# Optimization experiments

Measured on AMD Instinct MI355X. Metric: run time of the kernel, lower is better.

Reference implementation:

```python
import jax, jax.numpy as jnp
import numpy as np

N_HEADS = 16
D_MODEL = 2048
DK = D_MODEL // N_HEADS
SEQ = 2048


def setup_inputs() -> dict:
    key = jax.random.key(0)
    ks = jax.random.split(key, 11)
    s = 0.02
    return {
        "query": jax.random.normal(ks[0], (SEQ, D_MODEL), jnp.float32),
        "key": jax.random.normal(ks[1], (SEQ, D_MODEL), jnp.float32),
        "value": jax.random.normal(ks[2], (SEQ, D_MODEL), jnp.float32),
        # per-head projection weights, stacked over heads: [H, d_model, dk]
        "Wq": jax.random.normal(ks[3], (N_HEADS, D_MODEL, DK), jnp.float32) * s,
        "bq": jnp.zeros((N_HEADS, DK), jnp.float32),
        "Wk": jax.random.normal(ks[4], (N_HEADS, D_MODEL, DK), jnp.float32) * s,
        "bk": jnp.zeros((N_HEADS, DK), jnp.float32),
        "Wv": jax.random.normal(ks[5], (N_HEADS, D_MODEL, DK), jnp.float32) * s,
        "bv": jnp.zeros((N_HEADS, DK), jnp.float32),
        # output projection: [H*dk, d_model]
        "Wo": jax.random.normal(ks[6], (N_HEADS * DK, D_MODEL), jnp.float32) * s,
        "bo": jnp.zeros((D_MODEL,), jnp.float32),
    }


def reference(query, key, value, Wq, bq, Wk, bk, Wv, bv, Wo, bo):
    # Per-head linear projections, batched over heads. q/k/v: [H, S, dk]
    q = jnp.einsum('sd,hdk->hsk', query, Wq) + bq[:, None, :]
    k = jnp.einsum('sd,hdk->hsk', key, Wk) + bk[:, None, :]
    v = jnp.einsum('sd,hdk->hsk', value, Wv) + bv[:, None, :]
    scale = jnp.sqrt(jnp.asarray(DK, q.dtype))
    # scores: [H, S_q, S_k]
    scores = jnp.einsum('hsk,htk->hst', q, k) / scale
    # Faithful to original: Softmax(dim=0) on each 2D [S_q, S_k] matrix
    # -> normalize over the QUERY axis (axis=1 here).
    attn = jax.nn.softmax(scores, axis=1)
    heads = jnp.einsum('hst,htk->hsk', attn, v)  # [H, S, dk]
    # torch.cat(attentions, dim=1): [S, H*dk]
    concat = jnp.transpose(heads, (1, 0, 2)).reshape(SEQ, N_HEADS * DK)
    return concat @ Wo + bo
```

## Files before the change

kernel.cpp:

```cpp
#include <hip/hip_runtime.h>

#define SEQ 2048
#define DMODEL 2048
#define NHEADS 16
#define DKH 128

typedef __bf16 bf16;
typedef __attribute__((ext_vector_type(8))) __bf16 bf16x8;
typedef __attribute__((ext_vector_type(4))) __bf16 bf16x4;
typedef __attribute__((ext_vector_type(4))) float f32x4;

#define AS1 __attribute__((address_space(1)))
#define AS3 __attribute__((address_space(3)))

__device__ __forceinline__ void async_copy16(const void* g, void* l) {
  __builtin_amdgcn_global_load_lds((AS1 void*)(unsigned long long)g,
                                   (AS3 void*)l, 16, 0, 0);
}

__device__ __forceinline__ int swz(int chunk, int row) {
  return (chunk ^ (row & 7)) << 3;
}
__device__ __forceinline__ int swz16(int chunk, int row) {
  return (chunk ^ (row & 15)) << 3;
}

template <typename OutT, bool BIAS>
__global__ __launch_bounds__(256) void gemm_bt(
    const bf16* __restrict__ A, const bf16* __restrict__ B,
    const float* __restrict__ bias, OutT* __restrict__ C,
    int M, int N, int K, int lda, int ldb, int ldo, float scale,
    long long sA, long long sB, long long sC, long long sBias) {
  A += (long long)blockIdx.z * sA;
  B += (long long)blockIdx.z * sB;
  C += (long long)blockIdx.z * sC;
  const float* biasp = BIAS ? (bias + (long long)blockIdx.z * sBias) : nullptr;

  const int m0 = blockIdx.y * 128;
  const int n0 = blockIdx.x * 128;

  __shared__ __align__(16) bf16 As[128 * 64];
  __shared__ __align__(16) bf16 Bs[128 * 64];

  const int tid = threadIdx.x;
  const int wave = tid >> 6;
  const int lane = tid & 63;
  const int srow = wave * 8 + (lane >> 3);
  const int scol = ((lane & 7) ^ (lane >> 3)) * 8;
  const int wr = (wave >> 1) * 64;
  const int wc = (wave & 1) * 64;
  const int lr = lane & 15;
  const int quad = lane >> 4;

  const bf16* ag = A + (long long)(m0 + srow) * lda + scol;
  const bf16* bg = B + (long long)(n0 + srow) * ldb + scol;

  f32x4 acc[4][4];
#pragma unroll
  for (int i = 0; i < 4; ++i)
#pragma unroll
    for (int j = 0; j < 4; ++j) {
      acc[i][j][0] = 0.f; acc[i][j][1] = 0.f;
      acc[i][j][2] = 0.f; acc[i][j][3] = 0.f;
    }

  for (int kt = 0; kt < K; kt += 64) {
#pragma unroll
    for (int i = 0; i < 4; ++i) {
      async_copy16(ag + kt + (long long)i * 32 * lda, As + (i * 32 + wave * 8) * 64);
      async_copy16(bg + kt + (long long)i * 32 * ldb, Bs + (i * 32 + wave * 8) * 64);
    }
    __syncthreads();
#pragma unroll
    for (int kk = 0; kk < 64; kk += 32) {
      bf16x8 af[4], bfr[4];
#pragma unroll
      for (int i = 0; i < 4; ++i) {
        const int ra = wr + i * 16 + lr;
        const int rb = wc + i * 16 + lr;
        af[i]  = *(const bf16x8*)(As + ra * 64 + swz((kk >> 3) + quad, ra));
        bfr[i] = *(const bf16x8*)(Bs + rb * 64 + swz((kk >> 3) + quad, rb));
      }
#pragma unroll
      for (int i = 0; i < 4; ++i)
#pragma unroll
        for (int j = 0; j < 4; ++j)
          acc[i][j] = __builtin_amdgcn_mfma_f32_16x16x32_bf16(af[i], bfr[j], acc[i][j], 0, 0, 0);
    }
    __syncthreads();
  }

#pragma unroll
  for (int j = 0; j < 4; ++j) {
    const int n = n0 + wc + j * 16 + lr;
    const float bv = BIAS ? biasp[n] : 0.f;
#pragma unroll
    for (int i = 0; i < 4; ++i) {
      const int mb = m0 + wr + i * 16 + quad * 4;
#pragma unroll
      for (int r = 0; r < 4; ++r)
        C[(long long)(mb + r) * ldo + n] = (OutT)(acc[i][j][r] * scale + bv);
    }
  }
}

template <typename OutT, bool BIAS>
__global__ __launch_bounds__(256) void gemm_bt64(
    const bf16* __restrict__ A, const bf16* __restrict__ B,
    const float* __restrict__ bias, OutT* __restrict__ C,
    int K, int lda, int ldb, int ldo, float scale,
    long long sA, long long sB, long long sC) {
  A += (long long)blockIdx.z * sA;
  B += (long long)blockIdx.z * sB;
  C += (long long)blockIdx.z * sC;

  const int m0 = blockIdx.y * 64;
  const int n0 = blockIdx.x * 128;

  __shared__ __align__(16) bf16 As[64 * 64];
  __shared__ __align__(16) bf16 Bs[128 * 64];

  const int tid = threadIdx.x;
  const int wave = tid >> 6;
  const int lane = tid & 63;
  const int srow = wave * 8 + (lane >> 3);
  const int scol = ((lane & 7) ^ (lane >> 3)) * 8;
  const int wr = (wave >> 1) * 32;
  const int wc = (wave & 1) * 64;
  const int lr = lane & 15;
  const int quad = lane >> 4;

  const bf16* ag = A + (long long)(m0 + srow) * lda + scol;
  const bf16* bg = B + (long long)(n0 + srow) * ldb + scol;

  f32x4 acc[2][4];
#pragma unroll
  for (int i = 0; i < 2; ++i)
#pragma unroll
    for (int j = 0; j < 4; ++j) {
      acc[i][j][0] = 0.f; acc[i][j][1] = 0.f;
      acc[i][j][2] = 0.f; acc[i][j][3] = 0.f;
    }

  for (int kt = 0; kt < K; kt += 64) {
#pragma unroll
    for (int i = 0; i < 2; ++i)
      async_copy16(ag + kt + (long long)i * 32 * lda, As + (i * 32 + wave * 8) * 64);
#pragma unroll
    for (int i = 0; i < 4; ++i)
      async_copy16(bg + kt + (long long)i * 32 * ldb, Bs + (i * 32 + wave * 8) * 64);
    __syncthreads();
#pragma unroll
    for (int kk = 0; kk < 64; kk += 32) {
      bf16x8 af[2], bfr[4];
#pragma unroll
      for (int i = 0; i < 2; ++i) {
        const int ra = wr + i * 16 + lr;
        af[i] = *(const bf16x8*)(As + ra * 64 + swz((kk >> 3) + quad, ra));
      }
#pragma unroll
      for (int j = 0; j < 4; ++j) {
        const int rb = wc + j * 16 + lr;
        bfr[j] = *(const bf16x8*)(Bs + rb * 64 + swz((kk >> 3) + quad, rb));
      }
#pragma unroll
      for (int i = 0; i < 2; ++i)
#pragma unroll
        for (int j = 0; j < 4; ++j)
          acc[i][j] = __builtin_amdgcn_mfma_f32_16x16x32_bf16(af[i], bfr[j], acc[i][j], 0, 0, 0);
    }
    __syncthreads();
  }

#pragma unroll
  for (int j = 0; j < 4; ++j) {
    const int n = n0 + wc + j * 16 + lr;
    const float bv = BIAS ? bias[n] : 0.f;
#pragma unroll
    for (int i = 0; i < 2; ++i) {
      const int mb = m0 + wr + i * 16 + quad * 4;
#pragma unroll
      for (int r = 0; r < 4; ++r)
        C[(long long)(mb + r) * ldo + n] = (OutT)(acc[i][j][r] * scale + bv);
    }
  }
}

__global__ __launch_bounds__(256) void qk_exp(
    const bf16* __restrict__ q, const bf16* __restrict__ k,
    bf16* __restrict__ E, float* __restrict__ lpart) {
  const int h = blockIdx.z;
  const int m0 = blockIdx.y * 128;
  const int nstrip = blockIdx.x * 512;
  const bf16* A = q + (long long)h * DKH;
  const bf16* B = k + (long long)h * DKH;
  bf16* C = E + (long long)h * SEQ * SEQ;

  __shared__ __align__(16) bf16 As[128 * 128];
  __shared__ __align__(16) bf16 Bs[64 * 128];

  const int tid = threadIdx.x;
  const int wave = tid >> 6;
  const int lane = tid & 63;
  const int wr = (wave >> 1) * 64;
  const int wc = (wave & 1) * 32;
  const int lr = lane & 15;
  const int quad = lane >> 4;
  const float scale = 0.08838834764831845f;

#pragma unroll
  for (int it = 0; it < 8; ++it) {
    const int row = wave * 32 + it * 4 + (lane >> 4);
    const int chunk = (lane & 15) ^ (row & 15);
    async_copy16(A + (long long)(m0 + row) * DMODEL + chunk * 8,
                 As + (wave * 32 + it * 4) * 128);
  }

  for (int nt = 0; nt < 8; ++nt) {
    if (nt) __syncthreads();
#pragma unroll
    for (int it = 0; it < 4; ++it) {
      const int row = wave * 16 + it * 4 + (lane >> 4);
      const int chunk = (lane & 15) ^ (row & 15);
      async_copy16(B + (long long)(nstrip + nt * 64 + row) * DMODEL + chunk * 8,
                   Bs + (wave * 16 + it * 4) * 128);
    }
    __syncthreads();

    f32x4 acc[4][2];
#pragma unroll
    for (int i = 0; i < 4; ++i)
#pragma unroll
      for (int j = 0; j < 2; ++j) {
        acc[i][j][0] = 0.f; acc[i][j][1] = 0.f;
        acc[i][j][2] = 0.f; acc[i][j][3] = 0.f;
      }

#pragma unroll
    for (int kk = 0; kk < 128; kk += 32) {
      bf16x8 af[4], bfr[2];
#pragma unroll
      for (int i = 0; i < 4; ++i) {
        const int ra = wr + i * 16 + lr;
        af[i] = *(const bf16x8*)(As + ra * 128 + swz16((kk >> 3) + quad, ra));
      }
#pragma unroll
      for (int j = 0; j < 2; ++j) {
        const int rb = wc + j * 16 + lr;
        bfr[j] = *(const bf16x8*)(Bs + rb * 128 + swz16((kk >> 3) + quad, rb));
      }
#pragma unroll
      for (int i = 0; i < 4; ++i)
#pragma unroll
        for (int j = 0; j < 2; ++j)
          acc[i][j] = __builtin_amdgcn_mfma_f32_16x16x32_bf16(af[i], bfr[j], acc[i][j], 0, 0, 0);
    }

#pragma unroll
    for (int j = 0; j < 2; ++j) {
      const int n = nstrip + nt * 64 + wc + j * 16 + lr;
      float l_loc = 0.f;
#pragma unroll
      for (int i = 0; i < 4; ++i) {
        const int mb = m0 + wr + i * 16 + quad * 4;
#pragma unroll
        for (int r = 0; r < 4; ++r) {
          bf16 ev = (bf16)__expf(acc[i][j][r] * scale);
          C[(long long)(mb + r) * SEQ + n] = ev;
          l_loc += (float)ev;
        }
      }
      l_loc += __shfl_xor(l_loc, 16, 64);
      l_loc += __shfl_xor(l_loc, 32, 64);
      if (quad == 0)
        lpart[((long long)h * 32 + blockIdx.y * 2 + (wave >> 1)) * SEQ + n] = l_loc;
    }
  }
}

__global__ void sm_sum(const float* __restrict__ lp, float* __restrict__ rvec) {
  const int i = blockIdx.x * 256 + threadIdx.x;
  const int h = i >> 11, t = i & (SEQ - 1);
  float l = 0.f;
#pragma unroll
  for (int rb = 0; rb < 32; ++rb)
    l += lp[((long long)h * 32 + rb) * SEQ + t];
  rvec[i] = 1.f / l;
}

__global__ void vscale(bf16* __restrict__ vt, const float* __restrict__ rvec) {
  const int cg = blockIdx.y;
  const int t0 = threadIdx.x * 8;
  const float* r = rvec + (cg >> 7) * SEQ;
  bf16x8 v = *(const bf16x8*)(vt + (long long)cg * SEQ + t0);
#pragma unroll
  for (int e = 0; e < 8; ++e) v[e] = (bf16)((float)v[e] * r[t0 + e]);
  *(bf16x8*)(vt + (long long)cg * SEQ + t0) = v;
}

__global__ __launch_bounds__(256) void prep(
    const float* __restrict__ q, const float* __restrict__ k,
    const float* __restrict__ v,
    const float* __restrict__ Wq, const float* __restrict__ Wk,
    const float* __restrict__ Wv, const float* __restrict__ Wo,
    const float* __restrict__ bq, const float* __restrict__ bk,
    const float* __restrict__ bv,
    bf16* __restrict__ Qb, bf16* __restrict__ Wt, bf16* __restrict__ Wot,
    float* __restrict__ biasQKV) {
  __shared__ float tile[32][33];
  const long long elems = (long long)SEQ * DMODEL;
  const int id = blockIdx.x;
  const int tid = threadIdx.x;

  if (id < 12288) {
    const float* src = (id < 4096) ? q : (id < 8192) ? k : v;
    const int t = id >> 12;
    const long long i = (long long)(id & 4095) * 1024 + tid * 4;
    const float4 vv = *(const float4*)(src + i);
    bf16x4 o;
    o[0] = (bf16)vv.x; o[1] = (bf16)vv.y; o[2] = (bf16)vv.z; o[3] = (bf16)vv.w;
    *(bf16x4*)(Qb + (long long)t * elems + i) = o;
    return;
  }
  const int tx = tid & 31, ty = tid >> 5;
  if (id < 24576) {
    const int rel = id - 12288;
    const int z = rel >> 8;
    const int inner = rel & 255;
    const int bx = inner & 3;
    const int by = inner >> 2;
    const int g = z >> 4, hh = z & 15;
    const float* in = (g == 0 ? Wq : (g == 1 ? Wk : Wv)) + (long long)hh * DMODEL * DKH;
    bf16* o = Wt + (long long)z * DMODEL * DKH;
    const int c0 = bx * 32, r0 = by * 32;
#pragma unroll
    for (int j = 0; j < 32; j += 8)
      tile[ty + j][tx] = in[(long long)(r0 + ty + j) * DKH + c0 + tx];
    __syncthreads();
#pragma unroll
    for (int j = 0; j < 32; j += 8)
      o[(long long)(c0 + ty + j) * DMODEL + r0 + tx] = (bf16)tile[tx][ty + j];
    return;
  }
  if (id < 28672) {
    const int rel = id - 24576;
    const int bx = rel & 63, by = rel >> 6;
    const int c0 = bx * 32, r0 = by * 32;
#pragma unroll
    for (int j = 0; j < 32; j += 8)
      tile[ty + j][tx] = Wo[(long long)(r0 + ty + j) * DMODEL + c0 + tx];
    __syncthreads();
#pragma unroll
    for (int j = 0; j < 32; j += 8)
      Wot[(long long)(c0 + ty + j) * DMODEL + r0 + tx] = (bf16)tile[tx][ty + j];
    return;
  }
  {
    const int i = (id - 28672) * 256 + tid;
    if (i < NHEADS * DKH) {
      biasQKV[i] = bq[i];
      biasQKV[NHEADS * DKH + i] = bk[i];
      biasQKV[2 * NHEADS * DKH + i] = bv[i];
    }
  }
}

__global__ void transpose_v(const bf16* __restrict__ in, bf16* __restrict__ out) {
  __shared__ float tile[32][33];
  const int c0 = blockIdx.x * 32, r0 = blockIdx.y * 32;
  const int tx = threadIdx.x, ty = threadIdx.y;
#pragma unroll
  for (int j = 0; j < 32; j += 8)
    tile[ty + j][tx] = (float)in[(long long)(r0 + ty + j) * DMODEL + c0 + tx];
  __syncthreads();
#pragma unroll
  for (int j = 0; j < 32; j += 8)
    out[(long long)(c0 + ty + j) * SEQ + r0 + tx] = (bf16)tile[tx][ty + j];
}

extern "C" void kernel_launch(void* const* d_in, const int* in_sizes, int n_in,
                              void* d_out, int out_size, void* d_ws, size_t ws_size,
                              hipStream_t stream) {
  const float* query = (const float*)d_in[0];
  const float* key_  = (const float*)d_in[1];
  const float* value = (const float*)d_in[2];
  const float* Wq = (const float*)d_in[3];
  const float* bq = (const float*)d_in[4];
  const float* Wk = (const float*)d_in[5];
  const float* bk = (const float*)d_in[6];
  const float* Wv = (const float*)d_in[7];
  const float* bv = (const float*)d_in[8];
  const float* Wo = (const float*)d_in[9];
  const float* bo = (const float*)d_in[10];
  float* out = (float*)d_out;

  const long long elems = (long long)SEQ * DMODEL;
  const long long SZB = elems * 2;

  char* ws = (char*)d_ws;
  bf16* Qb = (bf16*)ws;
  bf16* Wt = (bf16*)(ws + 3 * SZB);
  bf16* scores = (bf16*)ws;
  char* p = ws + (long long)NHEADS * SEQ * SEQ * 2;
  float* biasQKV = (float*)p; p += 32 * 1024;
  bf16* Wot   = (bf16*)p; p += SZB;
  bf16* qkv   = (bf16*)p; p += 3 * SZB;
  bf16* vt    = (bf16*)p; p += SZB;
  bf16* heads = (bf16*)p; p += SZB;
  float* lpart = (float*)p; p += (long long)NHEADS * 32 * SEQ * 4;
  float* rvec  = (float*)p; p += (long long)NHEADS * SEQ * 4;
  if ((size_t)(p - ws) > ws_size) return;

  prep<<<28680, 256, 0, stream>>>(query, key_, value, Wq, Wk, Wv, Wo,
                                  bq, bk, bv, Qb, Wt, Wot, biasQKV);

  gemm_bt<bf16, true><<<dim3(16, 16, 3), 256, 0, stream>>>(
      Qb, Wt, biasQKV, qkv, SEQ, DMODEL, DMODEL, DMODEL, DMODEL, DMODEL, 1.f,
      elems, elems, elems, (long long)DMODEL);

  transpose_v<<<dim3(DMODEL / 32, SEQ / 32), dim3(32, 8), 0, stream>>>(
      qkv + 2 * elems, vt);

  qk_exp<<<dim3(4, 16, NHEADS), 256, 0, stream>>>(qkv, qkv + elems, scores, lpart);

  sm_sum<<<NHEADS * SEQ / 256, 256, 0, stream>>>(lpart, rvec);

  vscale<<<dim3(1, DMODEL), 256, 0, stream>>>(vt, rvec);

  gemm_bt64<bf16, false><<<dim3(1, SEQ / 64, NHEADS), 256, 0, stream>>>(
      scores, vt, nullptr, heads, SEQ, SEQ, SEQ, DMODEL, 1.f,
      (long long)SEQ * SEQ, (long long)DKH * SEQ, (long long)DKH);

  gemm_bt64<float, true><<<dim3(DMODEL / 128, SEQ / 64, 1), 256, 0, stream>>>(
      heads, Wot, bo, out, DMODEL, DMODEL, DMODEL, DMODEL, 1.f, 0, 0, 0);
}
```

Measured before the change: 348.1 us.

## Widen QK tile, fuse softmax sum with V scaling, vectorize V transpose

The QK-exp kernel now processes 128-column B tiles per iteration instead of 64. This halves the number of barriers and load phases and gives each wave a 4x4 MFMA tile, at the cost of more LDS and more accumulator registers. The column-sum reduction and the V scaling are fused into one kernel that keeps reciprocals in shared memory, removing the rvec buffer and one launch. The V transpose uses 64x64 bf16 tiles with 16-byte vector loads and stores instead of scalar float tiles.

```diff
diff --git a/kernel.cpp b/kernel.cpp
--- a/kernel.cpp
+++ b/kernel.cpp
@@ -197,13 +197,13 @@
   bf16* C = E + (long long)h * SEQ * SEQ;
 
   __shared__ __align__(16) bf16 As[128 * 128];
-  __shared__ __align__(16) bf16 Bs[64 * 128];
+  __shared__ __align__(16) bf16 Bs[128 * 128];
 
   const int tid = threadIdx.x;
   const int wave = tid >> 6;
   const int lane = tid & 63;
   const int wr = (wave >> 1) * 64;
-  const int wc = (wave & 1) * 32;
+  const int wc = (wave & 1) * 64;
   const int lr = lane & 15;
   const int quad = lane >> 4;
   const float scale = 0.08838834764831845f;
@@ -216,49 +216,49 @@
                  As + (wave * 32 + it * 4) * 128);
   }
 
-  for (int nt = 0; nt < 8; ++nt) {
+  for (int nt = 0; nt < 4; ++nt) {
     if (nt) __syncthreads();
 #pragma unroll
-    for (int it = 0; it < 4; ++it) {
-      const int row = wave * 16 + it * 4 + (lane >> 4);
+    for (int it = 0; it < 8; ++it) {
+      const int row = wave * 32 + it * 4 + (lane >> 4);
       const int chunk = (lane & 15) ^ (row & 15);
-      async_copy16(B + (long long)(nstrip + nt * 64 + row) * DMODEL + chunk * 8,
-                   Bs + (wave * 16 + it * 4) * 128);
-    }
-    __syncthreads();
-
-    f32x4 acc[4][2];
+      async_copy16(B + (long long)(nstrip + nt * 128 + row) * DMODEL + chunk * 8,
+                   Bs + (wave * 32 + it * 4) * 128);
+    }
+    __syncthreads();
+
+    f32x4 acc[4][4];
 #pragma unroll
     for (int i = 0; i < 4; ++i)
 #pragma unroll
-      for (int j = 0; j < 2; ++j) {
+      for (int j = 0; j < 4; ++j) {
         acc[i][j][0] = 0.f; acc[i][j][1] = 0.f;
         acc[i][j][2] = 0.f; acc[i][j][3] = 0.f;
       }
 
 #pragma unroll
     for (int kk = 0; kk < 128; kk += 32) {
-      bf16x8 af[4], bfr[2];
+      bf16x8 af[4], bfr[4];
 #pragma unroll
       for (int i = 0; i < 4; ++i) {
         const int ra = wr + i * 16 + lr;
         af[i] = *(const bf16x8*)(As + ra * 128 + swz16((kk >> 3) + quad, ra));
       }
 #pragma unroll
-      for (int j = 0; j < 2; ++j) {
+      for (int j = 0; j < 4; ++j) {
         const int rb = wc + j * 16 + lr;
         bfr[j] = *(const bf16x8*)(Bs + rb * 128 + swz16((kk >> 3) + quad, rb));
       }
 #pragma unroll
       for (int i = 0; i < 4; ++i)
 #pragma unroll
-        for (int j = 0; j < 2; ++j)
+        for (int j = 0; j < 4; ++j)
           acc[i][j] = __builtin_amdgcn_mfma_f32_16x16x32_bf16(af[i], bfr[j], acc[i][j], 0, 0, 0);
     }
 
 #pragma unroll
-    for (int j = 0; j < 2; ++j) {
-      const int n = nstrip + nt * 64 + wc + j * 16 + lr;
+    for (int j = 0; j < 4; ++j) {
+      const int n = nstrip + nt * 128 + wc + j * 16 + lr;
       float l_loc = 0.f;
 #pragma unroll
       for (int i = 0; i < 4; ++i) {
@@ -278,24 +278,30 @@
   }
 }
 
-__global__ void sm_sum(const float* __restrict__ lp, float* __restrict__ rvec) {
-  const int i = blockIdx.x * 256 + threadIdx.x;
-  const int h = i >> 11, t = i & (SEQ - 1);
+__global__ __launch_bounds__(256) void sum_scale(
+    const float* __restrict__ lp, bf16* __restrict__ vt) {
+  __shared__ float rv[256];
+  const int h = blockIdx.y;
+  const int t0 = blockIdx.x * 256;
+  const int tid = threadIdx.x;
+
   float l = 0.f;
 #pragma unroll
   for (int rb = 0; rb < 32; ++rb)
-    l += lp[((long long)h * 32 + rb) * SEQ + t];
-  rvec[i] = 1.f / l;
-}
-
-__global__ void vscale(bf16* __restrict__ vt, const float* __restrict__ rvec) {
-  const int cg = blockIdx.y;
-  const int t0 = threadIdx.x * 8;
-  const float* r = rvec + (cg >> 7) * SEQ;
-  bf16x8 v = *(const bf16x8*)(vt + (long long)cg * SEQ + t0);
-#pragma unroll
-  for (int e = 0; e < 8; ++e) v[e] = (bf16)((float)v[e] * r[t0 + e]);
-  *(bf16x8*)(vt + (long long)cg * SEQ + t0) = v;
+    l += lp[((long long)h * 32 + rb) * SEQ + t0 + tid];
+  rv[tid] = 1.f / l;
+  __syncthreads();
+
+  const int tc = (tid & 31) * 8;
+  const int c0 = tid >> 5;
+#pragma unroll
+  for (int cc = 0; cc < 128; cc += 8) {
+    const long long row = (long long)(h * DKH + cc + c0) * SEQ + t0 + tc;
+    bf16x8 v = *(const bf16x8*)(vt + row);
+#pragma unroll
+    for (int e = 0; e < 8; ++e) v[e] = (bf16)((float)v[e] * rv[tc + e]);
+    *(bf16x8*)(vt + row) = v;
+  }
 }
 
 __global__ __launch_bounds__(256) void prep(
@@ -365,17 +371,28 @@
   }
 }
 
-__global__ void transpose_v(const bf16* __restrict__ in, bf16* __restrict__ out) {
-  __shared__ float tile[32][33];
-  const int c0 = blockIdx.x * 32, r0 = blockIdx.y * 32;
-  const int tx = threadIdx.x, ty = threadIdx.y;
-#pragma unroll
-  for (int j = 0; j < 32; j += 8)
-    tile[ty + j][tx] = (float)in[(long long)(r0 + ty + j) * DMODEL + c0 + tx];
+__global__ __launch_bounds__(256) void transpose_v(
+    const bf16* __restrict__ in, bf16* __restrict__ out) {
+  __shared__ bf16 tile[64][72];
+  const int c0 = blockIdx.x * 64, r0 = blockIdx.y * 64;
+  const int tid = threadIdx.x;
+  const int row = tid >> 3;
+  const int ch = (tid & 7) * 8;
+#pragma unroll
+  for (int p = 0; p < 2; ++p) {
+    const int r = row + p * 32;
+    *(bf16x8*)(&tile[r][ch]) =
+        *(const bf16x8*)(in + (long long)(r0 + r) * DMODEL + c0 + ch);
+  }
   __syncthreads();
 #pragma unroll
-  for (int j = 0; j < 32; j += 8)
-    out[(long long)(c0 + ty + j) * SEQ + r0 + tx] = (bf16)tile[tx][ty + j];
+  for (int p = 0; p < 2; ++p) {
+    const int c = row + p * 32;
+    bf16x8 v;
+#pragma unroll
+    for (int e = 0; e < 8; ++e) v[e] = tile[ch + e][c];
+    *(bf16x8*)(out + (long long)(c0 + c) * SEQ + r0 + ch) = v;
+  }
 }
 
 extern "C" void kernel_launch(void* const* d_in, const int* in_sizes, int n_in,
@@ -408,7 +425,6 @@
   bf16* vt    = (bf16*)p; p += SZB;
   bf16* heads = (bf16*)p; p += SZB;
   float* lpart = (float*)p; p += (long long)NHEADS * 32 * SEQ * 4;
-  float* rvec  = (float*)p; p += (long long)NHEADS * SEQ * 4;
   if ((size_t)(p - ws) > ws_size) return;
 
   prep<<<28680, 256, 0, stream>>>(query, key_, value, Wq, Wk, Wv, Wo,
@@ -418,14 +434,12 @@
       Qb, Wt, biasQKV, qkv, SEQ, DMODEL, DMODEL, DMODEL, DMODEL, DMODEL, 1.f,
       elems, elems, elems, (long long)DMODEL);
 
-  transpose_v<<<dim3(DMODEL / 32, SEQ / 32), dim3(32, 8), 0, stream>>>(
+  transpose_v<<<dim3(DMODEL / 64, SEQ / 64), 256, 0, stream>>>(
       qkv + 2 * elems, vt);
 
   qk_exp<<<dim3(4, 16, NHEADS), 256, 0, stream>>>(qkv, qkv + elems, scores, lpart);
 
-  sm_sum<<<NHEADS * SEQ / 256, 256, 0, stream>>>(lpart, rvec);
-
-  vscale<<<dim3(1, DMODEL), 256, 0, stream>>>(vt, rvec);
+  sum_scale<<<dim3(SEQ / 256, NHEADS), 256, 0, stream>>>(lpart, vt);
 
   gemm_bt64<bf16, false><<<dim3(1, SEQ / 64, NHEADS), 256, 0, stream>>>(
       scores, vt, nullptr, heads, SEQ, SEQ, SEQ, DMODEL, 1.f,
```

Result: no change. 354.1 us (+1.7%).
